# Kernel optimization log

Hardware: AMD Instinct MI355X
Metric: run time of the kernel (lower is better)

Reference implementation:

```python
import jax, jax.numpy as jnp
import numpy as np

B, N, D, OUT = 4, 4096, 2048, 2048
E, RANK, TOP_K = 8, 16, 2
ALPHA = 16.0
SCALING = ALPHA / RANK


def setup_inputs() -> dict:
    key = jax.random.key(0)
    k1, k2, k3, k4 = jax.random.split(key, 4)
    x = jax.random.normal(k1, (B, N, D), dtype=jnp.float32)
    weight = jax.random.normal(k2, (OUT, D), dtype=jnp.float32) * (1.0 / np.sqrt(D))
    router_w = jax.random.normal(k3, (E, D), dtype=jnp.float32) * 0.02
    experts_A = jax.random.normal(k4, (E, D, RANK), dtype=jnp.float32) * (1.0 / np.sqrt(RANK))
    # experts_B is zero-initialized in the module; use small random values so the
    # LoRA branch contributes non-trivially to the output for kernel testing.
    experts_B = jax.random.normal(jax.random.fold_in(key, 5), (E, RANK, OUT), dtype=jnp.float32) * 0.02
    return {"x": x, "weight": weight, "router_w": router_w,
            "experts_A": experts_A, "experts_B": experts_B}


def reference(x, weight, router_w, experts_A, experts_B):
    # base = F.linear(x, weight)  (no bias)
    base = jnp.einsum('bnd,od->bno', x, weight)
    # router logits: x @ W_r^T -> (B, N, E)
    logits = jnp.einsum('bnd,ed->bne', x, router_w)
    # top-k sparse routing: keep top-k logits, set rest to -inf, softmax
    topk_vals, topk_idx = jax.lax.top_k(logits, TOP_K)  # (B,N,K)
    keep = jax.nn.one_hot(topk_idx, E, dtype=jnp.bool_).any(axis=-2)  # (B,N,E)
    masked = jnp.where(keep, logits, -jnp.inf)
    router_weights = jax.nn.softmax(masked, axis=-1)  # (B,N,E)
    # per-expert low-rank down/up projection, weighted by router
    lora_down = jnp.einsum('bnd,edr->bner', x, experts_A)  # (B,N,E,rank)
    weighted = lora_down * router_weights[..., None]
    moe_out = jnp.einsum('bner,erd->bnd', weighted, experts_B)  # (B,N,OUT)
    return base + SCALING * moe_out
```

## Files before the change

kernel.cpp:

```cpp
#include <hip/hip_runtime.h>
#include <stdint.h>

#define D_DIM 2048
#define OUT_DIM 2048
#define NTOK 16384
#define SCALING 1.0f
#define NT_TILES 34

typedef unsigned short u16;
typedef __attribute__((ext_vector_type(8))) short s16x8;
typedef __attribute__((ext_vector_type(4))) float f32x4;

#define WZ_OFF  0u
#define AZ_OFF  8388608u
#define BZ_OFF  8912896u
#define CZ_OFF  9437184u
#define W8_OFF  13631488u
#define XB_OFF  14155776u
#define WS_BIG   81264640u

__device__ inline u16 f2bf(float f) {
  union { float f; uint32_t u; } v; v.f = f;
  uint32_t u = v.u;
  u += 0x7FFFu + ((u >> 16) & 1u);
  return (u16)(u >> 16);
}

__global__ __launch_bounds__(256) void k_prep_router(
    const float* __restrict__ W, const float* __restrict__ A,
    const float* __restrict__ Bf, const float* __restrict__ x,
    const float* __restrict__ rw,
    u16* __restrict__ Wz, u16* __restrict__ Az, u16* __restrict__ Bz,
    float* __restrict__ w8, u16* __restrict__ xb) {
  int bid = blockIdx.x;
  if (bid < 4096) {
    int idx = bid * 256 + threadIdx.x;
    int o  = idx >> 9;
    int k0 = (idx & 511) * 4;
    const float4 v = *(const float4*)&W[(size_t)o * D_DIM + k0];
    int s = (o & 7) << 3;
    int dst = (k0 & ~63) | ((k0 & 63) ^ s);
    uint32_t p0 = (uint32_t)f2bf(v.x) | ((uint32_t)f2bf(v.y) << 16);
    uint32_t p1 = (uint32_t)f2bf(v.z) | ((uint32_t)f2bf(v.w) << 16);
    *(uint2*)&Wz[(size_t)o * D_DIM + dst] = make_uint2(p0, p1);
    return;
  }
  if (bid < 5120) {
    int idx = (bid - 4096) * 256 + threadIdx.x;
    float v = A[idx];
    int r = idx & 15;
    int d = (idx >> 4) & 2047;
    int e = idx >> 15;
    int er = e * 16 + r;
    int s = (er & 7) << 3;
    int dst = (d & ~63) | ((d & 63) ^ s);
    Az[(size_t)er * D_DIM + dst] = f2bf(v);
    return;
  }
  if (bid < 6144) {
    int idx = (bid - 5120) * 256 + threadIdx.x;
    float v = Bf[idx];
    int er = idx >> 11;
    int o  = idx & 2047;
    int s = (o & 7) << 3;
    int dst = (er & 64) | ((er & 63) ^ s);
    Bz[(size_t)o * 128 + dst] = f2bf(v);
    return;
  }
  int lane = threadIdx.x & 63, wid = threadIdx.x >> 6;
  int t = (bid - 6144) * 4 + wid;
  const float* xr = x + (size_t)t * D_DIM;
  float4 xv[8];
#pragma unroll
  for (int j = 0; j < 8; ++j) xv[j] = *(const float4*)&xr[j * 256 + lane * 4];
  int s = (t & 7) << 3;
#pragma unroll
  for (int j = 0; j < 8; ++j) {
    int c4 = j * 256 + lane * 4;
    int dst = (c4 & ~63) | ((c4 & 63) ^ s);
    uint32_t p0 = (uint32_t)f2bf(xv[j].x) | ((uint32_t)f2bf(xv[j].y) << 16);
    uint32_t p1 = (uint32_t)f2bf(xv[j].z) | ((uint32_t)f2bf(xv[j].w) << 16);
    *(uint2*)&xb[(size_t)t * D_DIM + dst] = make_uint2(p0, p1);
  }
  float lg[8];
#pragma unroll
  for (int e = 0; e < 8; ++e) {
    float a = 0.f;
#pragma unroll
    for (int j = 0; j < 8; ++j) {
      float4 rv = *(const float4*)&rw[e * D_DIM + j * 256 + lane * 4];
      a = fmaf(xv[j].x, rv.x, a); a = fmaf(xv[j].y, rv.y, a);
      a = fmaf(xv[j].z, rv.z, a); a = fmaf(xv[j].w, rv.w, a);
    }
#pragma unroll
    for (int off = 32; off; off >>= 1) a += __shfl_xor(a, off, 64);
    lg[e] = a;
  }
  int i0 = 0;
#pragma unroll
  for (int e = 1; e < 8; ++e) if (lg[e] > lg[i0]) i0 = e;
  int i1 = (i0 == 0) ? 1 : 0;
#pragma unroll
  for (int e = 0; e < 8; ++e) if (e != i0 && lg[e] > lg[i1]) i1 = e;
  float e1 = expf(lg[i1] - lg[i0]);
  float inv = 1.f / (1.f + e1);
  float w0 = inv * SCALING, w1 = e1 * inv * SCALING;
  if (lane < 8)
    w8[(size_t)t * 8 + lane] = (lane == i0) ? w0 : (lane == i1) ? w1 : 0.f;
}

__global__ __launch_bounds__(256) void k_lora64(const u16* __restrict__ xb,
                                                const u16* __restrict__ Az,
                                                const float* __restrict__ w8,
                                                u16* __restrict__ Cz) {
  __shared__ u16 Alds[2][64 * 64];
  __shared__ u16 Blds[2][128 * 64];
  __shared__ float w8s[64 * 8];
  int tid = threadIdx.x, lane = tid & 63, wid = tid >> 6;
  int t0 = blockIdx.x * 64;
  w8s[tid] = w8[(size_t)t0 * 8 + tid];
  w8s[256 + tid] = w8[(size_t)t0 * 8 + 256 + tid];
  f32x4 acc[8];
#pragma unroll
  for (int n = 0; n < 8; ++n) acc[n] = (f32x4){0.f, 0.f, 0.f, 0.f};
  const int ce = (lane >> 4) * 8;

  auto stage = [&](int kc, int buf) {
    if (kc > 31) kc = 31;
#pragma unroll
    for (int i = 0; i < 2; ++i) {
      const u16* g = xb + (size_t)(t0 + i * 32 + (tid >> 3)) * D_DIM + kc * 64 + (tid & 7) * 8;
      __builtin_amdgcn_global_load_lds(
          (const __attribute__((address_space(1))) void*)g,
          (__attribute__((address_space(3))) void*)(&Alds[buf][0] + i * 2048 + tid * 8), 16, 0, 0);
    }
#pragma unroll
    for (int i = 0; i < 4; ++i) {
      const u16* g = Az + (size_t)(i * 32 + (tid >> 3)) * D_DIM + kc * 64 + (tid & 7) * 8;
      __builtin_amdgcn_global_load_lds(
          (const __attribute__((address_space(1))) void*)g,
          (__attribute__((address_space(3))) void*)(&Blds[buf][0] + i * 2048 + tid * 8), 16, 0, 0);
    }
  };

  stage(0, 0);
  asm volatile("s_waitcnt vmcnt(0)" ::: "memory");
  __builtin_amdgcn_s_barrier();
  for (int kc = 0; kc < 32; ++kc) {
    int cur = kc & 1;
    stage(kc + 1, cur ^ 1);
#pragma unroll
    for (int kk = 0; kk < 2; ++kk) {
      int ar = wid * 16 + (lane & 15);
      s16x8 af = *(const s16x8*)&Alds[cur][ar * 64 + ((ce + kk * 32) ^ ((ar & 7) << 3))];
#pragma unroll
      for (int nf = 0; nf < 8; ++nf) {
        int br = nf * 16 + (lane & 15);
        s16x8 bf = *(const s16x8*)&Blds[cur][br * 64 + ((ce + kk * 32) ^ ((br & 7) << 3))];
        acc[nf] = __builtin_amdgcn_mfma_f32_16x16x32_bf16(af, bf, acc[nf], 0, 0, 0);
      }
    }
    asm volatile("s_waitcnt vmcnt(0)" ::: "memory");
    __builtin_amdgcn_s_barrier();
  }
#pragma unroll
  for (int q = 0; q < 4; ++q) {
    int rloc = wid * 16 + (lane >> 4) * 4 + q;
#pragma unroll
    for (int nf = 0; nf < 8; ++nf) {
      int er = nf * 16 + (lane & 15);
      float v = acc[nf][q] * w8s[rloc * 8 + (er >> 4)];
      int dst = (er & 64) | ((er & 63) ^ ((rloc & 7) << 3));
      Cz[(size_t)(t0 + rloc) * 128 + dst] = f2bf(v);
    }
  }
}

__device__ inline void stg(int kt, int h, int t0, int o0,
                           const u16* __restrict__ xb, const u16* __restrict__ Wz,
                           const u16* __restrict__ Cz, const u16* __restrict__ Bz,
                           u16* AshP, u16* BshP, int tid) {
  if (kt >= NT_TILES) kt = NT_TILES - 1;
  int p = kt & 1;
  const u16* src; int ld; size_t r0; int c0; u16* dst;
  if (h < 2) {
    if (kt < 32) { src = xb; ld = D_DIM; c0 = kt * 64; }
    else         { src = Cz; ld = 128;   c0 = (kt - 32) * 64; }
    r0 = (size_t)t0 + h * 128;
    dst = AshP + p * 16384 + h * 8192;
  } else {
    if (kt < 32) { src = Wz; ld = D_DIM; c0 = kt * 64; }
    else         { src = Bz; ld = 128;   c0 = (kt - 32) * 64; }
    r0 = (size_t)o0 + (h - 2) * 128;
    dst = BshP + p * 16384 + (h - 2) * 8192;
  }
#pragma unroll
  for (int i = 0; i < 2; ++i) {
    const u16* g = src + (r0 + i * 64 + (tid >> 3)) * (size_t)ld + c0 + (tid & 7) * 8;
    __builtin_amdgcn_global_load_lds(
        (const __attribute__((address_space(1))) void*)g,
        (__attribute__((address_space(3))) void*)(dst + i * 4096 + tid * 8), 16, 0, 0);
  }
}

__device__ inline void read_af(const u16* buf, int rbase, int ce, s16x8 a[4][2]) {
#pragma unroll
  for (int i = 0; i < 4; ++i)
#pragma unroll
    for (int kk = 0; kk < 2; ++kk) {
      int r = rbase + i * 16;
      a[i][kk] = *(const s16x8*)&buf[r * 64 + ((ce + kk * 32) ^ ((r & 7) << 3))];
    }
}

__device__ inline void read_b4(const u16* buf, int rbase, int ce, s16x8 b[4][2]) {
#pragma unroll
  for (int i = 0; i < 4; ++i)
#pragma unroll
    for (int kk = 0; kk < 2; ++kk) {
      int r = rbase + i * 16;
      b[i][kk] = *(const s16x8*)&buf[r * 64 + ((ce + kk * 32) ^ ((r & 7) << 3))];
    }
}

template <int MFH>
__device__ inline void mfma_half(f32x4 acc[8][4], const s16x8 a[4][2],
                                 const s16x8 b[4][2]) {
#pragma unroll
  for (int i = 0; i < 4; ++i)
#pragma unroll
    for (int j = 0; j < 4; ++j)
#pragma unroll
      for (int kk = 0; kk < 2; ++kk)
        acc[MFH * 4 + i][j] = __builtin_amdgcn_mfma_f32_16x16x32_bf16(
            a[i][kk], b[j][kk], acc[MFH * 4 + i][j], 0, 0, 0);
}

__global__ __launch_bounds__(512, 2) void k_main8(const u16* __restrict__ xb,
                                                  const u16* __restrict__ Wz,
                                                  const u16* __restrict__ Cz,
                                                  const u16* __restrict__ Bz,
                                                  float* __restrict__ out) {
  __shared__ u16 Ash[2][16384];
  __shared__ u16 Bsh[2][16384];
  const int tid = threadIdx.x, lane = tid & 63;
  const int wid = tid >> 6, wm = wid >> 2, wn = wid & 3;
  int bid = blockIdx.x;
  int swz = (bid & 7) * 64 + (bid >> 3);
  int mt = swz >> 3, nt = swz & 7;
  int t0 = mt * 256, o0 = nt * 256;
  const int ce = (lane >> 4) * 8;
  const int arb = wm * 128 + (lane & 15);
  const int brb = wn * 64 + (lane & 15);
  u16* A0p = &Ash[0][0];
  u16* B0p = &Bsh[0][0];

  f32x4 acc[8][4];
#pragma unroll
  for (int m = 0; m < 8; ++m)
#pragma unroll
    for (int n = 0; n < 4; ++n) acc[m][n] = (f32x4){0.f, 0.f, 0.f, 0.f};
  s16x8 a[4][2], b[4][2];

#define STG(kt) do { stg(kt, 0, t0, o0, xb, Wz, Cz, Bz, A0p, B0p, tid); \
                     stg(kt, 1, t0, o0, xb, Wz, Cz, Bz, A0p, B0p, tid); \
                     stg(kt, 2, t0, o0, xb, Wz, Cz, Bz, A0p, B0p, tid); \
                     stg(kt, 3, t0, o0, xb, Wz, Cz, Bz, A0p, B0p, tid); } while (0)

  STG(0);
  STG(1);
  asm volatile("s_waitcnt vmcnt(8)" ::: "memory");
  __builtin_amdgcn_s_barrier();

  for (int kt = 0; kt < NT_TILES; ++kt) {
    const int p = kt & 1;
    const u16* Abuf = A0p + p * 16384;
    const u16* Bbuf = B0p + p * 16384;
    read_af(Abuf, arb, ce, a);
    read_b4(Bbuf, brb, ce, b);
    mfma_half<0>(acc, a, b);
    read_af(Abuf, arb + 64, ce, a);
    mfma_half<1>(acc, a, b);
    __builtin_amdgcn_s_barrier();
    STG(kt + 2);
    asm volatile("s_waitcnt vmcnt(8)" ::: "memory");
    __builtin_amdgcn_s_barrier();
  }
  asm volatile("s_waitcnt vmcnt(0) lgkmcnt(0)" ::: "memory");
#undef STG

#pragma unroll
  for (int mf = 0; mf < 8; ++mf)
#pragma unroll
    for (int q = 0; q < 4; ++q) {
      int row = t0 + wm * 128 + mf * 16 + (lane >> 4) * 4 + q;
#pragma unroll
      for (int nf = 0; nf < 4; ++nf) {
        int col = o0 + wn * 64 + nf * 16 + (lane & 15);
        out[(size_t)row * OUT_DIM + col] = acc[mf][nf][q];
      }
    }
}

extern "C" void kernel_launch(void* const* d_in, const int* in_sizes, int n_in,
                              void* d_out, int out_size, void* d_ws, size_t ws_size,
                              hipStream_t stream) {
  const float* x  = (const float*)d_in[0];
  const float* W  = (const float*)d_in[1];
  const float* rw = (const float*)d_in[2];
  const float* eA = (const float*)d_in[3];
  const float* eB = (const float*)d_in[4];
  float* out = (float*)d_out;
  char* ws = (char*)d_ws;
  if (ws_size < WS_BIG) return;

  u16*   Wz = (u16*)(ws + WZ_OFF);
  u16*   Az = (u16*)(ws + AZ_OFF);
  u16*   Bz = (u16*)(ws + BZ_OFF);
  u16*   Cz = (u16*)(ws + CZ_OFF);
  float* w8 = (float*)(ws + W8_OFF);
  u16*   xb = (u16*)(ws + XB_OFF);

  k_prep_router<<<10240, 256, 0, stream>>>(W, eA, eB, x, rw, Wz, Az, Bz, w8, xb);
  k_lora64<<<256, 256, 0, stream>>>(xb, Az, w8, Cz);
  k_main8<<<512, 512, 0, stream>>>(xb, Wz, Cz, Bz, out);
}
```

Baseline: 253.1 us.

## Use 32-wide K tiles with 4-stage LDS ring and register double-buffering

The main GEMM kernel now stages 32-column K slices into a four-buffer LDS ring, where it used to stage 64-column slices into two buffers. It alternates two register fragment sets so that LDS reads for the next slice overlap MFMAs on the current one. The bf16 swizzle changes to a 32-column XOR pattern applied consistently in prep, the LoRA kernel and the main kernel. LDS footprint stays the same and prefetch depth grows, but there are twice as many barriers per unit of K work.

```diff
diff --git a/kernel.cpp b/kernel.cpp
--- a/kernel.cpp
+++ b/kernel.cpp
@@ -5,7 +5,7 @@
 #define OUT_DIM 2048
 #define NTOK 16384
 #define SCALING 1.0f
-#define NT_TILES 34
+#define NT32 68
 
 typedef unsigned short u16;
 typedef __attribute__((ext_vector_type(8))) short s16x8;
@@ -24,6 +24,10 @@
   uint32_t u = v.u;
   u += 0x7FFFu + ((u >> 16) & 1u);
   return (u16)(u >> 16);
+}
+
+__device__ inline int swz32(int c, int row) {
+  return (c & ~31) | (((((c >> 3) & 3) ^ ((row >> 1) & 3))) << 3) | (c & 7);
 }
 
 __global__ __launch_bounds__(256) void k_prep_router(
@@ -38,8 +42,7 @@
     int o  = idx >> 9;
     int k0 = (idx & 511) * 4;
     const float4 v = *(const float4*)&W[(size_t)o * D_DIM + k0];
-    int s = (o & 7) << 3;
-    int dst = (k0 & ~63) | ((k0 & 63) ^ s);
+    int dst = swz32(k0, o);
     uint32_t p0 = (uint32_t)f2bf(v.x) | ((uint32_t)f2bf(v.y) << 16);
     uint32_t p1 = (uint32_t)f2bf(v.z) | ((uint32_t)f2bf(v.w) << 16);
     *(uint2*)&Wz[(size_t)o * D_DIM + dst] = make_uint2(p0, p1);
@@ -52,9 +55,7 @@
     int d = (idx >> 4) & 2047;
     int e = idx >> 15;
     int er = e * 16 + r;
-    int s = (er & 7) << 3;
-    int dst = (d & ~63) | ((d & 63) ^ s);
-    Az[(size_t)er * D_DIM + dst] = f2bf(v);
+    Az[(size_t)er * D_DIM + swz32(d, er)] = f2bf(v);
     return;
   }
   if (bid < 6144) {
@@ -62,9 +63,7 @@
     float v = Bf[idx];
     int er = idx >> 11;
     int o  = idx & 2047;
-    int s = (o & 7) << 3;
-    int dst = (er & 64) | ((er & 63) ^ s);
-    Bz[(size_t)o * 128 + dst] = f2bf(v);
+    Bz[(size_t)o * 128 + swz32(er, o)] = f2bf(v);
     return;
   }
   int lane = threadIdx.x & 63, wid = threadIdx.x >> 6;
@@ -73,11 +72,10 @@
   float4 xv[8];
 #pragma unroll
   for (int j = 0; j < 8; ++j) xv[j] = *(const float4*)&xr[j * 256 + lane * 4];
-  int s = (t & 7) << 3;
 #pragma unroll
   for (int j = 0; j < 8; ++j) {
     int c4 = j * 256 + lane * 4;
-    int dst = (c4 & ~63) | ((c4 & 63) ^ s);
+    int dst = swz32(c4, t);
     uint32_t p0 = (uint32_t)f2bf(xv[j].x) | ((uint32_t)f2bf(xv[j].y) << 16);
     uint32_t p1 = (uint32_t)f2bf(xv[j].z) | ((uint32_t)f2bf(xv[j].w) << 16);
     *(uint2*)&xb[(size_t)t * D_DIM + dst] = make_uint2(p0, p1);
@@ -113,8 +111,8 @@
                                                 const u16* __restrict__ Az,
                                                 const float* __restrict__ w8,
                                                 u16* __restrict__ Cz) {
-  __shared__ u16 Alds[2][64 * 64];
-  __shared__ u16 Blds[2][128 * 64];
+  __shared__ u16 Al[2][2][64 * 32];
+  __shared__ u16 Bl[2][2][128 * 32];
   __shared__ float w8s[64 * 8];
   int tid = threadIdx.x, lane = tid & 63, wid = tid >> 6;
   int t0 = blockIdx.x * 64;
@@ -123,40 +121,41 @@
   f32x4 acc[8];
 #pragma unroll
   for (int n = 0; n < 8; ++n) acc[n] = (f32x4){0.f, 0.f, 0.f, 0.f};
-  const int ce = (lane >> 4) * 8;
+  const int l15 = lane & 15;
+  const int gA = (lane >> 4) ^ ((l15 >> 1) & 3);
+  const int arow = tid >> 2, c8 = (tid & 3) * 8;
 
   auto stage = [&](int kc, int buf) {
     if (kc > 31) kc = 31;
 #pragma unroll
-    for (int i = 0; i < 2; ++i) {
-      const u16* g = xb + (size_t)(t0 + i * 32 + (tid >> 3)) * D_DIM + kc * 64 + (tid & 7) * 8;
+    for (int kk = 0; kk < 2; ++kk) {
+      const u16* ga = xb + (size_t)(t0 + arow) * D_DIM + kc * 64 + kk * 32 + c8;
       __builtin_amdgcn_global_load_lds(
-          (const __attribute__((address_space(1))) void*)g,
-          (__attribute__((address_space(3))) void*)(&Alds[buf][0] + i * 2048 + tid * 8), 16, 0, 0);
-    }
-#pragma unroll
-    for (int i = 0; i < 4; ++i) {
-      const u16* g = Az + (size_t)(i * 32 + (tid >> 3)) * D_DIM + kc * 64 + (tid & 7) * 8;
-      __builtin_amdgcn_global_load_lds(
-          (const __attribute__((address_space(1))) void*)g,
-          (__attribute__((address_space(3))) void*)(&Blds[buf][0] + i * 2048 + tid * 8), 16, 0, 0);
+          (const __attribute__((address_space(1))) void*)ga,
+          (__attribute__((address_space(3))) void*)(&Al[buf][kk][0] + tid * 8), 16, 0, 0);
+#pragma unroll
+      for (int i = 0; i < 2; ++i) {
+        const u16* gb = Az + (size_t)(i * 64 + arow) * D_DIM + kc * 64 + kk * 32 + c8;
+        __builtin_amdgcn_global_load_lds(
+            (const __attribute__((address_space(1))) void*)gb,
+            (__attribute__((address_space(3))) void*)(&Bl[buf][kk][0] + i * 2048 + tid * 8), 16, 0, 0);
+      }
     }
   };
 
   stage(0, 0);
   asm volatile("s_waitcnt vmcnt(0)" ::: "memory");
   __builtin_amdgcn_s_barrier();
+  const int aoff = (wid * 16 + l15) * 32 + gA * 8;
   for (int kc = 0; kc < 32; ++kc) {
     int cur = kc & 1;
     stage(kc + 1, cur ^ 1);
 #pragma unroll
     for (int kk = 0; kk < 2; ++kk) {
-      int ar = wid * 16 + (lane & 15);
-      s16x8 af = *(const s16x8*)&Alds[cur][ar * 64 + ((ce + kk * 32) ^ ((ar & 7) << 3))];
+      s16x8 af = *(const s16x8*)&Al[cur][kk][aoff];
 #pragma unroll
       for (int nf = 0; nf < 8; ++nf) {
-        int br = nf * 16 + (lane & 15);
-        s16x8 bf = *(const s16x8*)&Blds[cur][br * 64 + ((ce + kk * 32) ^ ((br & 7) << 3))];
+        s16x8 bf = *(const s16x8*)&Bl[cur][kk][(nf * 16 + l15) * 32 + gA * 8];
         acc[nf] = __builtin_amdgcn_mfma_f32_16x16x32_bf16(af, bf, acc[nf], 0, 0, 0);
       }
     }
@@ -168,126 +167,96 @@
     int rloc = wid * 16 + (lane >> 4) * 4 + q;
 #pragma unroll
     for (int nf = 0; nf < 8; ++nf) {
-      int er = nf * 16 + (lane & 15);
+      int er = nf * 16 + l15;
       float v = acc[nf][q] * w8s[rloc * 8 + (er >> 4)];
-      int dst = (er & 64) | ((er & 63) ^ ((rloc & 7) << 3));
-      Cz[(size_t)(t0 + rloc) * 128 + dst] = f2bf(v);
-    }
-  }
-}
-
-__device__ inline void stg(int kt, int h, int t0, int o0,
-                           const u16* __restrict__ xb, const u16* __restrict__ Wz,
-                           const u16* __restrict__ Cz, const u16* __restrict__ Bz,
-                           u16* AshP, u16* BshP, int tid) {
-  if (kt >= NT_TILES) kt = NT_TILES - 1;
-  int p = kt & 1;
-  const u16* src; int ld; size_t r0; int c0; u16* dst;
-  if (h < 2) {
-    if (kt < 32) { src = xb; ld = D_DIM; c0 = kt * 64; }
-    else         { src = Cz; ld = 128;   c0 = (kt - 32) * 64; }
-    r0 = (size_t)t0 + h * 128;
-    dst = AshP + p * 16384 + h * 8192;
-  } else {
-    if (kt < 32) { src = Wz; ld = D_DIM; c0 = kt * 64; }
-    else         { src = Bz; ld = 128;   c0 = (kt - 32) * 64; }
-    r0 = (size_t)o0 + (h - 2) * 128;
-    dst = BshP + p * 16384 + (h - 2) * 8192;
-  }
-#pragma unroll
-  for (int i = 0; i < 2; ++i) {
-    const u16* g = src + (r0 + i * 64 + (tid >> 3)) * (size_t)ld + c0 + (tid & 7) * 8;
-    __builtin_amdgcn_global_load_lds(
-        (const __attribute__((address_space(1))) void*)g,
-        (__attribute__((address_space(3))) void*)(dst + i * 4096 + tid * 8), 16, 0, 0);
-  }
-}
-
-__device__ inline void read_af(const u16* buf, int rbase, int ce, s16x8 a[4][2]) {
-#pragma unroll
-  for (int i = 0; i < 4; ++i)
-#pragma unroll
-    for (int kk = 0; kk < 2; ++kk) {
-      int r = rbase + i * 16;
-      a[i][kk] = *(const s16x8*)&buf[r * 64 + ((ce + kk * 32) ^ ((r & 7) << 3))];
-    }
-}
-
-__device__ inline void read_b4(const u16* buf, int rbase, int ce, s16x8 b[4][2]) {
-#pragma unroll
-  for (int i = 0; i < 4; ++i)
-#pragma unroll
-    for (int kk = 0; kk < 2; ++kk) {
-      int r = rbase + i * 16;
-      b[i][kk] = *(const s16x8*)&buf[r * 64 + ((ce + kk * 32) ^ ((r & 7) << 3))];
-    }
-}
-
-template <int MFH>
-__device__ inline void mfma_half(f32x4 acc[8][4], const s16x8 a[4][2],
-                                 const s16x8 b[4][2]) {
-#pragma unroll
-  for (int i = 0; i < 4; ++i)
-#pragma unroll
-    for (int j = 0; j < 4; ++j)
-#pragma unroll
-      for (int kk = 0; kk < 2; ++kk)
-        acc[MFH * 4 + i][j] = __builtin_amdgcn_mfma_f32_16x16x32_bf16(
-            a[i][kk], b[j][kk], acc[MFH * 4 + i][j], 0, 0, 0);
-}
-
-__global__ __launch_bounds__(512, 2) void k_main8(const u16* __restrict__ xb,
-                                                  const u16* __restrict__ Wz,
-                                                  const u16* __restrict__ Cz,
-                                                  const u16* __restrict__ Bz,
-                                                  float* __restrict__ out) {
-  __shared__ u16 Ash[2][16384];
-  __shared__ u16 Bsh[2][16384];
+      Cz[(size_t)(t0 + rloc) * 128 + swz32(er, rloc)] = f2bf(v);
+    }
+  }
+}
+
+__global__ __launch_bounds__(512, 2) void k_main32(const u16* __restrict__ xb,
+                                                   const u16* __restrict__ Wz,
+                                                   const u16* __restrict__ Cz,
+                                                   const u16* __restrict__ Bz,
+                                                   float* __restrict__ out) {
+  __shared__ u16 AL[4][8192];
+  __shared__ u16 BL[4][8192];
   const int tid = threadIdx.x, lane = tid & 63;
   const int wid = tid >> 6, wm = wid >> 2, wn = wid & 3;
   int bid = blockIdx.x;
   int swz = (bid & 7) * 64 + (bid >> 3);
   int mt = swz >> 3, nt = swz & 7;
   int t0 = mt * 256, o0 = nt * 256;
-  const int ce = (lane >> 4) * 8;
-  const int arb = wm * 128 + (lane & 15);
-  const int brb = wn * 64 + (lane & 15);
-  u16* A0p = &Ash[0][0];
-  u16* B0p = &Bsh[0][0];
+  const int l15 = lane & 15;
+  const int gA = (lane >> 4) ^ ((l15 >> 1) & 3);
+  const int aoff = (wm * 128 + l15) * 32 + gA * 8;
+  const int boff = (wn * 64 + l15) * 32 + gA * 8;
+  const int srow = tid >> 2, sc8 = (tid & 3) * 8;
 
   f32x4 acc[8][4];
 #pragma unroll
   for (int m = 0; m < 8; ++m)
 #pragma unroll
     for (int n = 0; n < 4; ++n) acc[m][n] = (f32x4){0.f, 0.f, 0.f, 0.f};
-  s16x8 a[4][2], b[4][2];
-
-#define STG(kt) do { stg(kt, 0, t0, o0, xb, Wz, Cz, Bz, A0p, B0p, tid); \
-                     stg(kt, 1, t0, o0, xb, Wz, Cz, Bz, A0p, B0p, tid); \
-                     stg(kt, 2, t0, o0, xb, Wz, Cz, Bz, A0p, B0p, tid); \
-                     stg(kt, 3, t0, o0, xb, Wz, Cz, Bz, A0p, B0p, tid); } while (0)
-
-  STG(0);
-  STG(1);
-  asm volatile("s_waitcnt vmcnt(8)" ::: "memory");
+  s16x8 aA[8], bA[4], aB[8], bB[4];
+
+  auto stg = [&](int t, int bufi) {
+    if (t > NT32 - 1) t = NT32 - 1;
+    const u16 *sa, *sb; int lda, ldb, ca;
+    if (t < 64) { sa = xb; lda = D_DIM; sb = Wz; ldb = D_DIM; ca = t * 32; }
+    else        { sa = Cz; lda = 128;   sb = Bz; ldb = 128;   ca = (t - 64) * 32; }
+#pragma unroll
+    for (int i = 0; i < 2; ++i) {
+      const u16* g = sa + (size_t)(t0 + i * 128 + srow) * lda + ca + sc8;
+      __builtin_amdgcn_global_load_lds(
+          (const __attribute__((address_space(1))) void*)g,
+          (__attribute__((address_space(3))) void*)(&AL[bufi][0] + i * 4096 + tid * 8), 16, 0, 0);
+    }
+#pragma unroll
+    for (int i = 0; i < 2; ++i) {
+      const u16* g = sb + (size_t)(o0 + i * 128 + srow) * ldb + ca + sc8;
+      __builtin_amdgcn_global_load_lds(
+          (const __attribute__((address_space(1))) void*)g,
+          (__attribute__((address_space(3))) void*)(&BL[bufi][0] + i * 4096 + tid * 8), 16, 0, 0);
+    }
+  };
+
+#define RD(av, bv, bufi) do {                                           \
+    const u16* ap_ = &AL[bufi][aoff];                                   \
+    const u16* bp_ = &BL[bufi][boff];                                   \
+    _Pragma("unroll") for (int i_ = 0; i_ < 8; ++i_)                    \
+      av[i_] = *(const s16x8*)(ap_ + i_ * 512);                         \
+    _Pragma("unroll") for (int j_ = 0; j_ < 4; ++j_)                    \
+      bv[j_] = *(const s16x8*)(bp_ + j_ * 512);                         \
+  } while (0)
+
+#define MM(av, bv) do {                                                 \
+    _Pragma("unroll") for (int mf_ = 0; mf_ < 8; ++mf_)                 \
+      _Pragma("unroll") for (int nf_ = 0; nf_ < 4; ++nf_)               \
+        acc[mf_][nf_] = __builtin_amdgcn_mfma_f32_16x16x32_bf16(        \
+            av[mf_], bv[nf_], acc[mf_][nf_], 0, 0, 0);                  \
+  } while (0)
+
+  stg(0, 0); stg(1, 1); stg(2, 2);
+  asm volatile("s_waitcnt vmcnt(4)" ::: "memory");
   __builtin_amdgcn_s_barrier();
-
-  for (int kt = 0; kt < NT_TILES; ++kt) {
-    const int p = kt & 1;
-    const u16* Abuf = A0p + p * 16384;
-    const u16* Bbuf = B0p + p * 16384;
-    read_af(Abuf, arb, ce, a);
-    read_b4(Bbuf, brb, ce, b);
-    mfma_half<0>(acc, a, b);
-    read_af(Abuf, arb + 64, ce, a);
-    mfma_half<1>(acc, a, b);
+  RD(aA, bA, 0);
+
+  for (int jj = 0; jj < NT32; jj += 2) {
+    RD(aB, bB, (jj + 1) & 3);
+    MM(aA, bA);
+    stg(jj + 3, (jj + 3) & 3);
+    asm volatile("s_waitcnt vmcnt(4)" ::: "memory");
     __builtin_amdgcn_s_barrier();
-    STG(kt + 2);
-    asm volatile("s_waitcnt vmcnt(8)" ::: "memory");
+    RD(aA, bA, (jj + 2) & 3);
+    MM(aB, bB);
+    stg(jj + 4, (jj + 4) & 3);
+    asm volatile("s_waitcnt vmcnt(4)" ::: "memory");
     __builtin_amdgcn_s_barrier();
   }
   asm volatile("s_waitcnt vmcnt(0) lgkmcnt(0)" ::: "memory");
-#undef STG
+#undef RD
+#undef MM
 
 #pragma unroll
   for (int mf = 0; mf < 8; ++mf)
@@ -296,7 +265,7 @@
       int row = t0 + wm * 128 + mf * 16 + (lane >> 4) * 4 + q;
 #pragma unroll
       for (int nf = 0; nf < 4; ++nf) {
-        int col = o0 + wn * 64 + nf * 16 + (lane & 15);
+        int col = o0 + wn * 64 + nf * 16 + l15;
         out[(size_t)row * OUT_DIM + col] = acc[mf][nf][q];
       }
     }
@@ -323,5 +292,5 @@
 
   k_prep_router<<<10240, 256, 0, stream>>>(W, eA, eB, x, rw, Wz, Az, Bz, w8, xb);
   k_lora64<<<256, 256, 0, stream>>>(xb, Az, w8, Cz);
-  k_main8<<<512, 512, 0, stream>>>(xb, Wz, Cz, Bz, out);
-}
+  k_main32<<<512, 512, 0, stream>>>(xb, Wz, Cz, Bz, out);
+}
```

Measured after the change: 243.9 us. -3.6%, faster.
